# Kernel optimization log

Hardware: AMD Instinct MI355X
Metric: run time of the kernel (lower is better)

Reference implementation:

```python
import jax, jax.numpy as jnp
import numpy as np

N_NODES = 100000
N_EDGES = 1600000
IN_DIM = 64
HID = 32
OUT_DIM = 40


def setup_inputs() -> dict:
    key = jax.random.key(0)
    ks = jax.random.split(key, 9)
    x = jax.random.normal(ks[0], (N_NODES, IN_DIM), dtype=jnp.float32)
    edge_index = jax.random.randint(ks[1], (2, N_EDGES), 0, N_NODES, dtype=jnp.int64)
    # Xavier-ish scaled params (PyG SAGEConv: lin_l with bias, lin_r without)
    def glorot(k, shape):
        lim = float(np.sqrt(6.0 / (shape[0] + shape[1])))
        return jax.random.uniform(k, shape, jnp.float32, -lim, lim)
    W1l = glorot(ks[2], (IN_DIM, HID))
    b1 = jnp.zeros((HID,), jnp.float32)
    W1r = glorot(ks[3], (IN_DIM, HID))
    W2l = glorot(ks[4], (HID, HID))
    b2 = jnp.zeros((HID,), jnp.float32)
    W2r = glorot(ks[5], (HID, HID))
    w = glorot(ks[6], (HID, OUT_DIM))
    return {"x": x, "edge_index": edge_index, "W1l": W1l, "b1": b1,
            "W1r": W1r, "W2l": W2l, "b2": b2, "W2r": W2r, "w": w}


def reference(x, edge_index, W1l, b1, W1r, W2l, b2, W2r, w):
    src = edge_index[0]
    dst = edge_index[1]
    n = x.shape[0]
    # in-degree (for mean aggregation), clamp to avoid div-by-zero
    deg = jax.ops.segment_sum(jnp.ones((src.shape[0],), x.dtype), dst,
                              num_segments=n)
    inv_deg = 1.0 / jnp.maximum(deg, 1.0)  # [N]

    def sage_conv(h, Wl, b, Wr):
        # gather source features, scatter-mean to destinations
        agg = jax.ops.segment_sum(h[src], dst, num_segments=n)  # [N, d]
        agg = agg * inv_deg[:, None]
        return agg @ Wl + b + h @ Wr

    h = jax.nn.relu(sage_conv(x, W1l, b1, W1r))
    h = jax.nn.relu(sage_conv(h, W2l, b2, W2r))
    return h @ w
```

## Files before the change

kernel.cpp:

```cpp
#include <hip/hip_runtime.h>
#include <hip/hip_bf16.h>

#define N_NODES 100000
#define N_EDGES 1600000
#define IN_DIM 64
#define HID 32
#define OUT_DIM 40

#define NBUK 196
#define BCAP 9216
#define BIN_TILE 8192

__device__ __forceinline__ float bf2f(unsigned short u) {
    return __uint_as_float(((unsigned int)u) << 16);
}
__device__ __forceinline__ unsigned short f2bf(float f) {
    unsigned int u = __float_as_uint(f);
    u = (u + 0x7fffu + ((u >> 16) & 1u)) >> 16;
    return (unsigned short)u;
}

__global__ void detect_i64(const int* __restrict__ p, int* __restrict__ flagp,
                           int* __restrict__ cnt) {
    __shared__ int s_any;
    if (threadIdx.x == 0) s_any = 0;
    __syncthreads();
    cnt[threadIdx.x] = 0;
    int any = 0;
    for (int i = threadIdx.x; i < 2048; i += blockDim.x) any |= p[2 * i + 1];
    if (any) atomicOr(&s_any, 1);
    __syncthreads();
    if (threadIdx.x == 0) *flagp = (s_any == 0) ? 1 : 0;
}

__device__ __forceinline__ int load_idx(const void* ei, int i64, long long pos) {
    if (i64) return (int)((const long long*)ei)[pos];
    return ((const int*)ei)[pos];
}

__global__ __launch_bounds__(1024) void bin_kernel(const void* __restrict__ ei,
                                                   const int* __restrict__ flagp,
                                                   int* __restrict__ cnt,
                                                   int* __restrict__ binned) {
    __shared__ int lcount[NBUK];
    __shared__ int lscan[NBUK + 1];
    __shared__ int lcur[NBUK];
    __shared__ int lbase[NBUK];
    __shared__ int wsum16[16];
    __shared__ int stage[BIN_TILE];
    const int t = threadIdx.x;
    if (t < NBUK) lcount[t] = 0;
    __syncthreads();

    const long long e0 = (long long)blockIdx.x * BIN_TILE;
    const int i64 = *flagp;
    int vv[8], bb[8];
#pragma unroll
    for (int k = 0; k < 8; ++k) {
        const long long e = e0 + (long long)k * 1024 + t;
        if (e < N_EDGES) {
            const int s = load_idx(ei, i64, e);
            const int d = load_idx(ei, i64, N_EDGES + e);
            bb[k] = d >> 9;
            vv[k] = (s << 9) | (d & 511);
            atomicAdd(&lcount[bb[k]], 1);
        } else {
            bb[k] = -1;
        }
    }
    __syncthreads();
    const int ival = (t < NBUK) ? lcount[t] : 0;
    const int lane = t & 63;
    const int wid = t >> 6;
    int sv = ival;
#pragma unroll
    for (int off = 1; off < 64; off <<= 1) {
        const int nn = __shfl_up(sv, off, 64);
        if (lane >= off) sv += nn;
    }
    if (lane == 63) wsum16[wid] = sv;
    __syncthreads();
    if (t == 0) {
        int acc = 0;
#pragma unroll
        for (int i = 0; i < 16; ++i) {
            const int x = wsum16[i];
            wsum16[i] = acc;
            acc += x;
        }
    }
    __syncthreads();
    const int incl = sv + wsum16[wid];
    if (t < NBUK) lscan[t] = incl - ival;
    if (t == NBUK - 1) lscan[NBUK] = incl;
    __syncthreads();
    if (t < NBUK) {
        const int c = lcount[t];
        lbase[t] = t * BCAP + (c > 0 ? atomicAdd(&cnt[t], c) : 0);
        lcur[t] = lscan[t];
    }
    __syncthreads();
#pragma unroll
    for (int k = 0; k < 8; ++k) {
        if (bb[k] >= 0) {
            const int pos = atomicAdd(&lcur[bb[k]], 1);
            stage[pos] = vv[k];
        }
    }
    __syncthreads();
    const int total = lscan[NBUK];
    for (int j = t; j < total; j += 1024) {
        int lo = 0, hi = NBUK;
        while (hi - lo > 1) {
            const int mid = (lo + hi) >> 1;
            if (lscan[mid] <= j) lo = mid;
            else hi = mid;
        }
        binned[lbase[lo] + (j - lscan[lo])] = stage[j];
    }
}

__global__ __launch_bounds__(512) void sort_kernel(const int* __restrict__ cnt,
                                                   const int* __restrict__ binned,
                                                   int* __restrict__ rowstart,
                                                   int* __restrict__ csr) {
    __shared__ int counts[512];
    __shared__ int wsum8[8];
    __shared__ int sbase;
    const int b = blockIdx.x;
    const int t = threadIdx.x;
    const int lane = t & 63;
    const int wid = t >> 6;
    int r = (t < b) ? cnt[t] : 0;
#pragma unroll
    for (int off = 1; off < 64; off <<= 1) r += __shfl_xor(r, off, 64);
    if (lane == 0) wsum8[wid] = r;
    __syncthreads();
    if (t == 0) {
        int s = 0;
#pragma unroll
        for (int i = 0; i < 8; ++i) s += wsum8[i];
        sbase = s;
        if (b == 0) rowstart[N_NODES] = N_EDGES;
    }
    __syncthreads();
    const int base = sbase;
    const int n = cnt[b];
    const int* __restrict__ bin = binned + (long long)b * BCAP;
    counts[t] = 0;
    __syncthreads();
    for (int i = t; i < n; i += 512) atomicAdd(&counts[bin[i] & 511], 1);
    __syncthreads();
    const int v = counts[t];
    int sv = v;
#pragma unroll
    for (int off = 1; off < 64; off <<= 1) {
        const int nn = __shfl_up(sv, off, 64);
        if (lane >= off) sv += nn;
    }
    if (lane == 63) wsum8[wid] = sv;
    __syncthreads();
    if (t == 0) {
        int acc = 0;
#pragma unroll
        for (int i = 0; i < 8; ++i) {
            const int x = wsum8[i];
            wsum8[i] = acc;
            acc += x;
        }
    }
    __syncthreads();
    const int excl = sv + wsum8[wid] - v;
    const int node = b * 512 + t;
    if (node < N_NODES) rowstart[node] = base + excl;
    counts[t] = excl;
    __syncthreads();
    for (int i = t; i < n; i += 512) {
        const int vv = bin[i];
        const int pos = atomicAdd(&counts[vv & 511], 1);
        csr[base + pos] = vv >> 9;
    }
}

__global__ __launch_bounds__(256) void lin1_kernel(
    const float* __restrict__ x, const float* __restrict__ Wl,
    const float* __restrict__ Wr, unsigned short* __restrict__ yl,
    unsigned short* __restrict__ yr) {
    __shared__ float sWl[IN_DIM * HID];
    __shared__ float sWr[IN_DIM * HID];
    __shared__ float sX[64 * IN_DIM];
    const int t = threadIdx.x;
    for (int i = t; i < IN_DIM * HID; i += 256) {
        sWl[i] = Wl[i];
        sWr[i] = Wr[i];
    }
    const long long r0 = (long long)blockIdx.x * 64;
    const int nrows = (int)((N_NODES - r0) < 64 ? (N_NODES - r0) : 64);
    const float4* xv = (const float4*)(x + r0 * IN_DIM);
    float4* sXv = (float4*)sX;
    for (int i = t; i < nrows * 16; i += 256) sXv[i] = xv[i];
    __syncthreads();

    const int c = t & 31;
    const int rbase = (t >> 5) * 8;
    float al[8] = {0, 0, 0, 0, 0, 0, 0, 0};
    float ar[8] = {0, 0, 0, 0, 0, 0, 0, 0};
    for (int k = 0; k < IN_DIM; k += 4) {
        const float wl0 = sWl[(k + 0) * HID + c];
        const float wl1 = sWl[(k + 1) * HID + c];
        const float wl2 = sWl[(k + 2) * HID + c];
        const float wl3 = sWl[(k + 3) * HID + c];
        const float wr0 = sWr[(k + 0) * HID + c];
        const float wr1 = sWr[(k + 1) * HID + c];
        const float wr2 = sWr[(k + 2) * HID + c];
        const float wr3 = sWr[(k + 3) * HID + c];
#pragma unroll
        for (int r = 0; r < 8; ++r) {
            const float4 xv4 = *(const float4*)&sX[(rbase + r) * IN_DIM + k];
            al[r] = fmaf(xv4.x, wl0, al[r]);
            al[r] = fmaf(xv4.y, wl1, al[r]);
            al[r] = fmaf(xv4.z, wl2, al[r]);
            al[r] = fmaf(xv4.w, wl3, al[r]);
            ar[r] = fmaf(xv4.x, wr0, ar[r]);
            ar[r] = fmaf(xv4.y, wr1, ar[r]);
            ar[r] = fmaf(xv4.z, wr2, ar[r]);
            ar[r] = fmaf(xv4.w, wr3, ar[r]);
        }
    }
    __syncthreads();
    unsigned short* sB = (unsigned short*)sX;
#pragma unroll
    for (int r = 0; r < 8; ++r) {
        if (rbase + r < nrows) {
            sB[(rbase + r) * HID + c] = f2bf(al[r]);
            sB[2048 + (rbase + r) * HID + c] = f2bf(ar[r]);
        }
    }
    __syncthreads();
    uint4* dl = (uint4*)(yl + r0 * HID);
    uint4* dr = (uint4*)(yr + r0 * HID);
    const uint4* sl = (const uint4*)sB;
    const uint4* sr = (const uint4*)(sB + 2048);
    for (int i = t; i < nrows * 4; i += 256) {
        dl[i] = sl[i];
        dr[i] = sr[i];
    }
}

__device__ __forceinline__ void gather_node8(
    const int* __restrict__ csr, const unsigned short* __restrict__ yl,
    const unsigned short* __restrict__ yr, const float* __restrict__ b,
    int node, int start, int end, int q, float* sHrow) {
    float ax = 0.f, ay = 0.f, az = 0.f, aw = 0.f;
    const unsigned short* yq = yl + q * 4;
    int e = start;
    for (; e + 7 < end; e += 8) {
        int s[8];
#pragma unroll
        for (int j = 0; j < 8; ++j) s[j] = csr[e + j];
        ushort4 v[8];
#pragma unroll
        for (int j = 0; j < 8; ++j)
            v[j] = *(const ushort4*)(yq + (long long)s[j] * HID);
#pragma unroll
        for (int j = 0; j < 8; ++j) {
            ax += bf2f(v[j].x);
            ay += bf2f(v[j].y);
            az += bf2f(v[j].z);
            aw += bf2f(v[j].w);
        }
    }
    if (e + 3 < end) {
        int s[4];
#pragma unroll
        for (int j = 0; j < 4; ++j) s[j] = csr[e + j];
#pragma unroll
        for (int j = 0; j < 4; ++j) {
            const ushort4 v = *(const ushort4*)(yq + (long long)s[j] * HID);
            ax += bf2f(v.x);
            ay += bf2f(v.y);
            az += bf2f(v.z);
            aw += bf2f(v.w);
        }
        e += 4;
    }
    if (e + 1 < end) {
        const int s0 = csr[e];
        const int s1 = csr[e + 1];
        const ushort4 v0 = *(const ushort4*)(yq + (long long)s0 * HID);
        const ushort4 v1 = *(const ushort4*)(yq + (long long)s1 * HID);
        ax += bf2f(v0.x) + bf2f(v1.x);
        ay += bf2f(v0.y) + bf2f(v1.y);
        az += bf2f(v0.z) + bf2f(v1.z);
        aw += bf2f(v0.w) + bf2f(v1.w);
        e += 2;
    }
    if (e < end) {
        const int s0 = csr[e];
        const ushort4 v0 = *(const ushort4*)(yq + (long long)s0 * HID);
        ax += bf2f(v0.x);
        ay += bf2f(v0.y);
        az += bf2f(v0.z);
        aw += bf2f(v0.w);
    }
    const float inv = 1.0f / fmaxf((float)(end - start), 1.0f);
    const ushort4 rv = *(const ushort4*)(yr + (long long)node * HID + q * 4);
    const float4 bb = *(const float4*)(b + q * 4);
    sHrow[q * 4 + 0] = fmaxf(fmaf(ax, inv, bb.x) + bf2f(rv.x), 0.f);
    sHrow[q * 4 + 1] = fmaxf(fmaf(ay, inv, bb.y) + bf2f(rv.y), 0.f);
    sHrow[q * 4 + 2] = fmaxf(fmaf(az, inv, bb.z) + bf2f(rv.z), 0.f);
    sHrow[q * 4 + 3] = fmaxf(fmaf(aw, inv, bb.w) + bf2f(rv.w), 0.f);
}

__global__ __launch_bounds__(256) void gather_lin2(
    const int* __restrict__ rowstart, const int* __restrict__ csr,
    const unsigned short* __restrict__ yl, const unsigned short* __restrict__ yr,
    const float* __restrict__ b, const float* __restrict__ W2l,
    const float* __restrict__ W2r, unsigned short* __restrict__ y2l,
    unsigned short* __restrict__ y2r) {
    __shared__ float sH[32 * 33];
    __shared__ float sW2l[HID * HID];
    __shared__ float sW2r[HID * HID];
    __shared__ int srow[33];
    const int t = threadIdx.x;
    for (int i = t; i < HID * HID; i += 256) {
        sW2l[i] = W2l[i];
        sW2r[i] = W2r[i];
    }
    const int n0 = blockIdx.x * 32;
    if (t < 33) srow[t] = rowstart[n0 + t];
    __syncthreads();

    const int ln = t >> 3;
    const int q = t & 7;
    const int node = n0 + ln;
    gather_node8(csr, yl, yr, b, node, srow[ln], srow[ln + 1], q, &sH[ln * 33]);
    __syncthreads();

    float l0 = 0, l1 = 0, l2 = 0, l3 = 0, m0 = 0, m1 = 0, m2 = 0, m3 = 0;
#pragma unroll
    for (int k = 0; k < HID; ++k) {
        const float hk = sH[ln * 33 + k];
        const float4 wl = *(const float4*)&sW2l[k * HID + q * 4];
        const float4 wr = *(const float4*)&sW2r[k * HID + q * 4];
        l0 = fmaf(hk, wl.x, l0);
        l1 = fmaf(hk, wl.y, l1);
        l2 = fmaf(hk, wl.z, l2);
        l3 = fmaf(hk, wl.w, l3);
        m0 = fmaf(hk, wr.x, m0);
        m1 = fmaf(hk, wr.y, m1);
        m2 = fmaf(hk, wr.z, m2);
        m3 = fmaf(hk, wr.w, m3);
    }
    ushort4 pl, pr;
    pl.x = f2bf(l0);
    pl.y = f2bf(l1);
    pl.z = f2bf(l2);
    pl.w = f2bf(l3);
    pr.x = f2bf(m0);
    pr.y = f2bf(m1);
    pr.z = f2bf(m2);
    pr.w = f2bf(m3);
    *(ushort4*)(y2l + (long long)node * HID + q * 4) = pl;
    *(ushort4*)(y2r + (long long)node * HID + q * 4) = pr;
}

__global__ __launch_bounds__(256) void gather_out(
    const int* __restrict__ rowstart, const int* __restrict__ csr,
    const unsigned short* __restrict__ yl, const unsigned short* __restrict__ yr,
    const float* __restrict__ b, const float* __restrict__ w,
    float* __restrict__ out) {
    __shared__ float sH[32 * 33];
    __shared__ float sW[HID * OUT_DIM];
    __shared__ int srow[33];
    const int t = threadIdx.x;
    for (int i = t; i < HID * OUT_DIM; i += 256) sW[i] = w[i];
    const int n0 = blockIdx.x * 32;
    if (t < 33) srow[t] = rowstart[n0 + t];
    __syncthreads();

    const int ln = t >> 3;
    const int q = t & 7;
    const int node = n0 + ln;
    gather_node8(csr, yl, yr, b, node, srow[ln], srow[ln + 1], q, &sH[ln * 33]);
    __syncthreads();

    float o[5] = {0, 0, 0, 0, 0};
#pragma unroll
    for (int k = 0; k < HID; ++k) {
        const float hk = sH[ln * 33 + k];
#pragma unroll
        for (int j = 0; j < 5; ++j)
            o[j] = fmaf(hk, sW[k * OUT_DIM + q + 8 * j], o[j]);
    }
#pragma unroll
    for (int j = 0; j < 5; ++j) out[(long long)node * OUT_DIM + q + 8 * j] = o[j];
}

extern "C" void kernel_launch(void* const* d_in, const int* in_sizes, int n_in,
                              void* d_out, int out_size, void* d_ws,
                              size_t ws_size, hipStream_t stream) {
    const float* x = (const float*)d_in[0];
    const void* ei = d_in[1];
    const float* W1l = (const float*)d_in[2];
    const float* b1 = (const float*)d_in[3];
    const float* W1r = (const float*)d_in[4];
    const float* W2l = (const float*)d_in[5];
    const float* b2 = (const float*)d_in[6];
    const float* W2r = (const float*)d_in[7];
    const float* w = (const float*)d_in[8];
    float* out = (float*)d_out;

    int* ip = (int*)d_ws;
    int* flagp = ip;
    int* cnt = ip + 64;
    int* rowstart = ip + 320;
    int* csr = rowstart + 100032;
    unsigned short* Y1l = (unsigned short*)(csr + N_EDGES);
    unsigned short* Y1r = Y1l + (long long)N_NODES * HID;
    unsigned short* Y2l = Y1r + (long long)N_NODES * HID;
    unsigned short* Y2r = Y2l + (long long)N_NODES * HID;
    int* binned = (int*)Y2l;

    detect_i64<<<1, 256, 0, stream>>>((const int*)ei, flagp, cnt);

    bin_kernel<<<(N_EDGES + BIN_TILE - 1) / BIN_TILE, 1024, 0, stream>>>(
        ei, flagp, cnt, binned);
    sort_kernel<<<NBUK, 512, 0, stream>>>(cnt, binned, rowstart, csr);

    lin1_kernel<<<(N_NODES + 63) / 64, 256, 0, stream>>>(x, W1l, W1r, Y1l, Y1r);

    gather_lin2<<<(N_NODES + 31) / 32, 256, 0, stream>>>(rowstart, csr, Y1l,
                                                         Y1r, b1, W2l, W2r,
                                                         Y2l, Y2r);

    gather_out<<<(N_NODES + 31) / 32, 256, 0, stream>>>(rowstart, csr, Y2l, Y2r,
                                                        b2, w, out);
}
```

Baseline: 122.3 us.

## Merge CSR sort and first linear layer into one heterogeneous launch

Combines the per-bucket CSR sort and the layer-1 dense projection into a single kernel. The first NBUK blocks run the sort and the remaining blocks each compute 64 rows of x@W1l and x@W1r. The two pieces of work are independent, so one launch lets them overlap and removes a kernel boundary. Lin blocks now use 512 threads with 4 rows per thread instead of 256 threads with 8 rows, and shared memory is a single 32KB union sized for the larger of the two paths, which may change occupancy.

```diff
diff --git a/kernel.cpp b/kernel.cpp
--- a/kernel.cpp
+++ b/kernel.cpp
@@ -10,6 +10,7 @@
 #define NBUK 196
 #define BCAP 9216
 #define BIN_TILE 8192
+#define NLIN 1563
 
 __device__ __forceinline__ float bf2f(unsigned short u) {
     return __uint_as_float(((unsigned int)u) << 16);
@@ -120,130 +121,130 @@
     }
 }
 
-__global__ __launch_bounds__(512) void sort_kernel(const int* __restrict__ cnt,
-                                                   const int* __restrict__ binned,
-                                                   int* __restrict__ rowstart,
-                                                   int* __restrict__ csr) {
-    __shared__ int counts[512];
-    __shared__ int wsum8[8];
-    __shared__ int sbase;
-    const int b = blockIdx.x;
-    const int t = threadIdx.x;
-    const int lane = t & 63;
-    const int wid = t >> 6;
-    int r = (t < b) ? cnt[t] : 0;
-#pragma unroll
-    for (int off = 1; off < 64; off <<= 1) r += __shfl_xor(r, off, 64);
-    if (lane == 0) wsum8[wid] = r;
-    __syncthreads();
-    if (t == 0) {
-        int s = 0;
-#pragma unroll
-        for (int i = 0; i < 8; ++i) s += wsum8[i];
-        sbase = s;
-        if (b == 0) rowstart[N_NODES] = N_EDGES;
-    }
-    __syncthreads();
-    const int base = sbase;
-    const int n = cnt[b];
-    const int* __restrict__ bin = binned + (long long)b * BCAP;
-    counts[t] = 0;
-    __syncthreads();
-    for (int i = t; i < n; i += 512) atomicAdd(&counts[bin[i] & 511], 1);
-    __syncthreads();
-    const int v = counts[t];
-    int sv = v;
-#pragma unroll
-    for (int off = 1; off < 64; off <<= 1) {
-        const int nn = __shfl_up(sv, off, 64);
-        if (lane >= off) sv += nn;
-    }
-    if (lane == 63) wsum8[wid] = sv;
-    __syncthreads();
-    if (t == 0) {
-        int acc = 0;
-#pragma unroll
-        for (int i = 0; i < 8; ++i) {
-            const int x = wsum8[i];
-            wsum8[i] = acc;
-            acc += x;
-        }
-    }
-    __syncthreads();
-    const int excl = sv + wsum8[wid] - v;
-    const int node = b * 512 + t;
-    if (node < N_NODES) rowstart[node] = base + excl;
-    counts[t] = excl;
-    __syncthreads();
-    for (int i = t; i < n; i += 512) {
-        const int vv = bin[i];
-        const int pos = atomicAdd(&counts[vv & 511], 1);
-        csr[base + pos] = vv >> 9;
-    }
-}
-
-__global__ __launch_bounds__(256) void lin1_kernel(
+__global__ __launch_bounds__(512) void sortlin_kernel(
+    const int* __restrict__ cnt, const int* __restrict__ binned,
+    int* __restrict__ rowstart, int* __restrict__ csr,
     const float* __restrict__ x, const float* __restrict__ Wl,
     const float* __restrict__ Wr, unsigned short* __restrict__ yl,
     unsigned short* __restrict__ yr) {
-    __shared__ float sWl[IN_DIM * HID];
-    __shared__ float sWr[IN_DIM * HID];
-    __shared__ float sX[64 * IN_DIM];
+    __shared__ __align__(16) char smem[32768];
     const int t = threadIdx.x;
-    for (int i = t; i < IN_DIM * HID; i += 256) {
-        sWl[i] = Wl[i];
-        sWr[i] = Wr[i];
-    }
-    const long long r0 = (long long)blockIdx.x * 64;
-    const int nrows = (int)((N_NODES - r0) < 64 ? (N_NODES - r0) : 64);
-    const float4* xv = (const float4*)(x + r0 * IN_DIM);
-    float4* sXv = (float4*)sX;
-    for (int i = t; i < nrows * 16; i += 256) sXv[i] = xv[i];
-    __syncthreads();
-
-    const int c = t & 31;
-    const int rbase = (t >> 5) * 8;
-    float al[8] = {0, 0, 0, 0, 0, 0, 0, 0};
-    float ar[8] = {0, 0, 0, 0, 0, 0, 0, 0};
-    for (int k = 0; k < IN_DIM; k += 4) {
-        const float wl0 = sWl[(k + 0) * HID + c];
-        const float wl1 = sWl[(k + 1) * HID + c];
-        const float wl2 = sWl[(k + 2) * HID + c];
-        const float wl3 = sWl[(k + 3) * HID + c];
-        const float wr0 = sWr[(k + 0) * HID + c];
-        const float wr1 = sWr[(k + 1) * HID + c];
-        const float wr2 = sWr[(k + 2) * HID + c];
-        const float wr3 = sWr[(k + 3) * HID + c];
-#pragma unroll
-        for (int r = 0; r < 8; ++r) {
-            const float4 xv4 = *(const float4*)&sX[(rbase + r) * IN_DIM + k];
-            al[r] = fmaf(xv4.x, wl0, al[r]);
-            al[r] = fmaf(xv4.y, wl1, al[r]);
-            al[r] = fmaf(xv4.z, wl2, al[r]);
-            al[r] = fmaf(xv4.w, wl3, al[r]);
-            ar[r] = fmaf(xv4.x, wr0, ar[r]);
-            ar[r] = fmaf(xv4.y, wr1, ar[r]);
-            ar[r] = fmaf(xv4.z, wr2, ar[r]);
-            ar[r] = fmaf(xv4.w, wr3, ar[r]);
-        }
-    }
-    __syncthreads();
-    unsigned short* sB = (unsigned short*)sX;
-#pragma unroll
-    for (int r = 0; r < 8; ++r) {
-        if (rbase + r < nrows) {
-            sB[(rbase + r) * HID + c] = f2bf(al[r]);
-            sB[2048 + (rbase + r) * HID + c] = f2bf(ar[r]);
-        }
-    }
-    __syncthreads();
-    uint4* dl = (uint4*)(yl + r0 * HID);
-    uint4* dr = (uint4*)(yr + r0 * HID);
-    const uint4* sl = (const uint4*)sB;
-    const uint4* sr = (const uint4*)(sB + 2048);
-    for (int i = t; i < nrows * 4; i += 256) {
-        dl[i] = sl[i];
-        dr[i] = sr[i];
+
+    if (blockIdx.x < NBUK) {
+        int* counts = (int*)smem;
+        int* wsum8 = counts + 512;
+        int* sbasep = wsum8 + 8;
+        const int b = blockIdx.x;
+        const int lane = t & 63;
+        const int wid = t >> 6;
+        int r = (t < b) ? cnt[t] : 0;
+#pragma unroll
+        for (int off = 1; off < 64; off <<= 1) r += __shfl_xor(r, off, 64);
+        if (lane == 0) wsum8[wid] = r;
+        __syncthreads();
+        if (t == 0) {
+            int s = 0;
+#pragma unroll
+            for (int i = 0; i < 8; ++i) s += wsum8[i];
+            *sbasep = s;
+            if (b == 0) rowstart[N_NODES] = N_EDGES;
+        }
+        __syncthreads();
+        const int base = *sbasep;
+        const int n = cnt[b];
+        const int* __restrict__ bin = binned + (long long)b * BCAP;
+        counts[t] = 0;
+        __syncthreads();
+        for (int i = t; i < n; i += 512) atomicAdd(&counts[bin[i] & 511], 1);
+        __syncthreads();
+        const int v = counts[t];
+        int sv = v;
+#pragma unroll
+        for (int off = 1; off < 64; off <<= 1) {
+            const int nn = __shfl_up(sv, off, 64);
+            if (lane >= off) sv += nn;
+        }
+        if (lane == 63) wsum8[wid] = sv;
+        __syncthreads();
+        if (t == 0) {
+            int acc = 0;
+#pragma unroll
+            for (int i = 0; i < 8; ++i) {
+                const int xq = wsum8[i];
+                wsum8[i] = acc;
+                acc += xq;
+            }
+        }
+        __syncthreads();
+        const int excl = sv + wsum8[wid] - v;
+        const int node = b * 512 + t;
+        if (node < N_NODES) rowstart[node] = base + excl;
+        counts[t] = excl;
+        __syncthreads();
+        for (int i = t; i < n; i += 512) {
+            const int vv = bin[i];
+            const int pos = atomicAdd(&counts[vv & 511], 1);
+            csr[base + pos] = vv >> 9;
+        }
+    } else {
+        float* sWl = (float*)smem;
+        float* sWr = sWl + 2048;
+        float* sX = sWl + 4096;
+        for (int i = t; i < IN_DIM * HID; i += 512) {
+            sWl[i] = Wl[i];
+            sWr[i] = Wr[i];
+        }
+        const long long r0 = (long long)(blockIdx.x - NBUK) * 64;
+        const int nrows = (int)((N_NODES - r0) < 64 ? (N_NODES - r0) : 64);
+        const float4* xv = (const float4*)(x + r0 * IN_DIM);
+        float4* sXv = (float4*)sX;
+        for (int i = t; i < nrows * 16; i += 512) sXv[i] = xv[i];
+        __syncthreads();
+
+        const int c = t & 31;
+        const int rbase = (t >> 5) * 4;
+        float al[4] = {0, 0, 0, 0};
+        float ar[4] = {0, 0, 0, 0};
+        for (int k = 0; k < IN_DIM; k += 4) {
+            const float wl0 = sWl[(k + 0) * HID + c];
+            const float wl1 = sWl[(k + 1) * HID + c];
+            const float wl2 = sWl[(k + 2) * HID + c];
+            const float wl3 = sWl[(k + 3) * HID + c];
+            const float wr0 = sWr[(k + 0) * HID + c];
+            const float wr1 = sWr[(k + 1) * HID + c];
+            const float wr2 = sWr[(k + 2) * HID + c];
+            const float wr3 = sWr[(k + 3) * HID + c];
+#pragma unroll
+            for (int rr = 0; rr < 4; ++rr) {
+                const float4 xv4 = *(const float4*)&sX[(rbase + rr) * IN_DIM + k];
+                al[rr] = fmaf(xv4.x, wl0, al[rr]);
+                al[rr] = fmaf(xv4.y, wl1, al[rr]);
+                al[rr] = fmaf(xv4.z, wl2, al[rr]);
+                al[rr] = fmaf(xv4.w, wl3, al[rr]);
+                ar[rr] = fmaf(xv4.x, wr0, ar[rr]);
+                ar[rr] = fmaf(xv4.y, wr1, ar[rr]);
+                ar[rr] = fmaf(xv4.z, wr2, ar[rr]);
+                ar[rr] = fmaf(xv4.w, wr3, ar[rr]);
+            }
+        }
+        __syncthreads();
+        unsigned short* sB = (unsigned short*)sX;
+#pragma unroll
+        for (int rr = 0; rr < 4; ++rr) {
+            if (rbase + rr < nrows) {
+                sB[(rbase + rr) * HID + c] = f2bf(al[rr]);
+                sB[2048 + (rbase + rr) * HID + c] = f2bf(ar[rr]);
+            }
+        }
+        __syncthreads();
+        uint4* dl = (uint4*)(yl + r0 * HID);
+        uint4* dr = (uint4*)(yr + r0 * HID);
+        const uint4* sl = (const uint4*)sB;
+        const uint4* sr = (const uint4*)(sB + 2048);
+        for (int i = t; i < nrows * 4; i += 512) {
+            dl[i] = sl[i];
+            dr[i] = sr[i];
+        }
     }
 }
 
@@ -426,9 +427,9 @@
 
     bin_kernel<<<(N_EDGES + BIN_TILE - 1) / BIN_TILE, 1024, 0, stream>>>(
         ei, flagp, cnt, binned);
-    sort_kernel<<<NBUK, 512, 0, stream>>>(cnt, binned, rowstart, csr);
-
-    lin1_kernel<<<(N_NODES + 63) / 64, 256, 0, stream>>>(x, W1l, W1r, Y1l, Y1r);
+
+    sortlin_kernel<<<NBUK + NLIN, 512, 0, stream>>>(cnt, binned, rowstart, csr,
+                                                    x, W1l, W1r, Y1l, Y1r);
 
     gather_lin2<<<(N_NODES + 31) / 32, 256, 0, stream>>>(rowstart, csr, Y1l,
                                                          Y1r, b1, W2l, W2r,
```

Result: slower. 426.1 us (+248.6%).
